# Optimization experiments

Measured on AMD Instinct MI355X. Metric: run time of the kernel, lower is better.

Reference implementation:

```python
import jax, jax.numpy as jnp
import numpy as np

VOCAB = 50257
CH = 1024          # c_hidden_size = hidden_size(1020) + class_num(4)
LAT = 128
T = 1024
EOS = 1


def setup_inputs() -> dict:
    key = jax.random.key(0)
    ks = jax.random.split(key, 12)
    s = 0.02
    # tokens in [2, VOCAB) so EOS only appears at the final position
    toks = jax.random.randint(ks[0], (T,), 2, VOCAB, dtype=jnp.int32)
    input_tensor = toks.at[-1].set(EOS)
    inp = {
        "input_tensor": input_tensor,
        "h0": jnp.zeros((1, 1, CH), jnp.float32),
        "c0": jnp.zeros((1, 1, CH), jnp.float32),
        "eps": jax.random.normal(ks[1], (1, 1, LAT), jnp.float32),
        "emb": jax.random.normal(ks[2], (VOCAB, CH), jnp.float32) * s,
        "W_ih": jax.random.normal(ks[3], (4 * CH, CH), jnp.float32) * s,
        "W_hh": jax.random.normal(ks[4], (4 * CH, CH), jnp.float32) * s,
        "b_ih": jax.random.normal(ks[5], (4 * CH,), jnp.float32) * s,
        "b_hh": jax.random.normal(ks[6], (4 * CH,), jnp.float32) * s,
        "W_mean": jax.random.normal(ks[7], (LAT, 2 * CH), jnp.float32) * s,
        "b_mean": jnp.zeros((LAT,), jnp.float32),
        "W_logv": jax.random.normal(ks[8], (LAT, 2 * CH), jnp.float32) * s,
        "b_logv": jnp.zeros((LAT,), jnp.float32),
    }
    return inp


def reference(input_tensor, h0, c0, eps, emb, W_ih, W_hh, b_ih, b_hh,
              W_mean, b_mean, W_logv, b_logv):
    Tlen = input_tensor.shape[0]
    eos_idx = jnp.argmax(input_tensor == EOS)           # first EOS position
    active = jnp.arange(Tlen) < eos_idx                 # steps taken before break
    x_all = emb[input_tensor]                            # [T, CH]

    def step(carry, inp):
        h, c = carry
        x, a = inp
        gates = x @ W_ih.T + b_ih + h @ W_hh.T + b_hh    # [4*CH]
        i, f, g, o = jnp.split(gates, 4)                 # PyTorch LSTM gate order
        c_new = jax.nn.sigmoid(f) * c + jax.nn.sigmoid(i) * jnp.tanh(g)
        h_new = jax.nn.sigmoid(o) * jnp.tanh(c_new)
        h = jnp.where(a, h_new, h)
        c = jnp.where(a, c_new, c)
        return (h, c), None

    (h, c), _ = jax.lax.scan(step, (h0.reshape(-1), c0.reshape(-1)), (x_all, active))
    hc = jnp.concatenate([h, c])                         # cat((h, c), dim=2) flattened
    mean = hc @ W_mean.T + b_mean
    logv = hc @ W_logv.T + b_logv
    z = eps.reshape(-1) * jnp.exp(0.5 * logv) + mean     # reparameterize
    shp = (1, 1, LAT)
    return z.reshape(shp), mean.reshape(shp), logv.reshape(shp)
```

## Files before the change

kernel.cpp:

```cpp
#include <hip/hip_runtime.h>
#include <cstdint>
#include <cstddef>

#define T_LEN 1024
#define CH    1024
#define NGATE 4096
#define LAT   128
#define NBLK  128

#define WS_HBUF  (16777216)
#define WS_HFIN  (16777216 + 16384)
#define WS_CFIN  (16777216 + 24576)

#define SWZ(j) ((j) ^ ((((j) >> 5) & 7) << 2))

__device__ __forceinline__ float sigmf(float x) { return 1.0f / (1.0f + expf(-x)); }

template <int CTRL, int RM>
__device__ __forceinline__ float dpp_add(float x) {
  int t = __builtin_amdgcn_update_dpp(0, __float_as_int(x), CTRL, RM, 0xf, true);
  return x + __int_as_float(t);
}

__device__ __forceinline__ float wave_sum63(float x) {
  x = dpp_add<0x111, 0xf>(x);
  x = dpp_add<0x112, 0xf>(x);
  x = dpp_add<0x114, 0xf>(x);
  x = dpp_add<0x118, 0xf>(x);
  x = dpp_add<0x142, 0xa>(x);
  x = dpp_add<0x143, 0xc>(x);
  return x;
}

__global__ __launch_bounds__(1024, 4) void lstm_k(const int* __restrict__ tok,
                                                  const float* __restrict__ h0,
                                                  const float* __restrict__ c0,
                                                  const float* __restrict__ eps,
                                                  const float* __restrict__ emb,
                                                  const float* __restrict__ Wih,
                                                  const float* __restrict__ Whh,
                                                  const float* __restrict__ bih,
                                                  const float* __restrict__ bhh,
                                                  const float* __restrict__ Wm,
                                                  const float* __restrict__ bm,
                                                  const float* __restrict__ Wl,
                                                  const float* __restrict__ bl,
                                                  unsigned long long* __restrict__ hbuf64,
                                                  unsigned long long* __restrict__ hfin64,
                                                  unsigned long long* __restrict__ cfin64,
                                                  float* __restrict__ out) {
  __shared__ float hs[1024];
  __shared__ float hcs[2048];
  __shared__ float4 gpart[16];
  __shared__ float rs[32];
  __shared__ int red[1024];

  const int tid = threadIdx.x;
  const int b = blockIdx.x;
  const int wv = tid >> 6;
  const int ln = tid & 63;
  const int dw = wv & 7;
  const int mb = (wv >> 3) * 2;
  const int kbase = ln * 16 + 4 * mb;
  const int hsw = SWZ(tid);
  const int swzmask = ((ln >> 1) & 7) << 2;
  const int idx0 = kbase ^ swzmask;
  const int idx1 = (kbase + 4) ^ swzmask;

  red[tid] = (tok[tid] == 1) ? tid : 0x7fffffff;
  __syncthreads();
  for (int s = 512; s > 0; s >>= 1) {
    if (tid < s) red[tid] = min(red[tid], red[tid + s]);
    __syncthreads();
  }
  const int e0 = red[0];
  const int eos = (e0 == 0x7fffffff) ? 0 : e0;
  __syncthreads();

  float4 w4[4][2];
  float4 wx[4][2];
#pragma unroll
  for (int q = 0; q < 4; q++) {
    const size_t roff = (size_t)(q * 1024 + b * 8 + dw) * CH + kbase;
    w4[q][0] = *(const float4*)(Whh + roff);
    w4[q][1] = *(const float4*)(Whh + roff + 4);
    wx[q][0] = *(const float4*)(Wih + roff);
    wx[q][1] = *(const float4*)(Wih + roff + 4);
  }

  float bias[4] = {0.f, 0.f, 0.f, 0.f};
  if (tid < 8) {
#pragma unroll
    for (int q = 0; q < 4; q++) {
      const int r = q * 1024 + b * 8 + tid;
      bias[q] = bih[r] + bhh[r];
    }
  }

  float hreg = 0.0f, creg = 0.0f;
  if (tid < 8) { hreg = h0[b * 8 + tid]; creg = c0[b * 8 + tid]; }

  for (int t = 0; t < eos; t++) {
    const int tokv = tok[t];
    const float* xrow = emb + (size_t)tokv * CH + kbase;
    const float4 x4a = *(const float4*)(xrow);
    const float4 x4b = *(const float4*)(xrow + 4);

    if (t == 0) {
      hs[hsw] = h0[tid];
    } else {
      const unsigned want = (unsigned)t;
      const unsigned long long* src = hbuf64 + (size_t)(t & 1) * 1024 + tid;
      unsigned long long v;
      do {
        v = __hip_atomic_load(src, __ATOMIC_RELAXED, __HIP_MEMORY_SCOPE_AGENT);
      } while ((unsigned)(v >> 32) != want);
      hs[hsw] = __uint_as_float((unsigned)(v & 0xffffffffu));
    }
    __syncthreads();

    float a0, a1, a2, a3;
    {
      a0 = wx[0][0].x * x4a.x + wx[0][0].y * x4a.y +
           wx[0][0].z * x4a.z + wx[0][0].w * x4a.w +
           wx[0][1].x * x4b.x + wx[0][1].y * x4b.y +
           wx[0][1].z * x4b.z + wx[0][1].w * x4b.w;
      a1 = wx[1][0].x * x4a.x + wx[1][0].y * x4a.y +
           wx[1][0].z * x4a.z + wx[1][0].w * x4a.w +
           wx[1][1].x * x4b.x + wx[1][1].y * x4b.y +
           wx[1][1].z * x4b.z + wx[1][1].w * x4b.w;
      a2 = wx[2][0].x * x4a.x + wx[2][0].y * x4a.y +
           wx[2][0].z * x4a.z + wx[2][0].w * x4a.w +
           wx[2][1].x * x4b.x + wx[2][1].y * x4b.y +
           wx[2][1].z * x4b.z + wx[2][1].w * x4b.w;
      a3 = wx[3][0].x * x4a.x + wx[3][0].y * x4a.y +
           wx[3][0].z * x4a.z + wx[3][0].w * x4a.w +
           wx[3][1].x * x4b.x + wx[3][1].y * x4b.y +
           wx[3][1].z * x4b.z + wx[3][1].w * x4b.w;
      const float4 h4a = *(const float4*)&hs[idx0];
      const float4 h4b = *(const float4*)&hs[idx1];
      a0 += w4[0][0].x * h4a.x; a0 += w4[0][0].y * h4a.y;
      a0 += w4[0][0].z * h4a.z; a0 += w4[0][0].w * h4a.w;
      a0 += w4[0][1].x * h4b.x; a0 += w4[0][1].y * h4b.y;
      a0 += w4[0][1].z * h4b.z; a0 += w4[0][1].w * h4b.w;
      a1 += w4[1][0].x * h4a.x; a1 += w4[1][0].y * h4a.y;
      a1 += w4[1][0].z * h4a.z; a1 += w4[1][0].w * h4a.w;
      a1 += w4[1][1].x * h4b.x; a1 += w4[1][1].y * h4b.y;
      a1 += w4[1][1].z * h4b.z; a1 += w4[1][1].w * h4b.w;
      a2 += w4[2][0].x * h4a.x; a2 += w4[2][0].y * h4a.y;
      a2 += w4[2][0].z * h4a.z; a2 += w4[2][0].w * h4a.w;
      a2 += w4[2][1].x * h4b.x; a2 += w4[2][1].y * h4b.y;
      a2 += w4[2][1].z * h4b.z; a2 += w4[2][1].w * h4b.w;
      a3 += w4[3][0].x * h4a.x; a3 += w4[3][0].y * h4a.y;
      a3 += w4[3][0].z * h4a.z; a3 += w4[3][0].w * h4a.w;
      a3 += w4[3][1].x * h4b.x; a3 += w4[3][1].y * h4b.y;
      a3 += w4[3][1].z * h4b.z; a3 += w4[3][1].w * h4b.w;
    }
    a0 = wave_sum63(a0);
    a1 = wave_sum63(a1);
    a2 = wave_sum63(a2);
    a3 = wave_sum63(a3);
    if (ln == 63) gpart[wv] = float4{a0, a1, a2, a3};
    __syncthreads();

    if (tid < 8) {
      const float4 g0 = gpart[tid];
      const float4 g1 = gpart[tid + 8];
      const float iv = g0.x + g1.x + bias[0];
      const float fv = g0.y + g1.y + bias[1];
      const float gg = g0.z + g1.z + bias[2];
      const float ov = g0.w + g1.w + bias[3];
      const float cn = sigmf(fv) * creg + sigmf(iv) * tanhf(gg);
      const float hn = sigmf(ov) * tanhf(cn);
      creg = cn; hreg = hn;
      const unsigned long long pv =
          ((unsigned long long)(unsigned)(t + 1) << 32) |
          (unsigned long long)__float_as_uint(hn);
      __hip_atomic_store(&hbuf64[(size_t)((t + 1) & 1) * 1024 + b * 8 + tid], pv,
                         __ATOMIC_RELAXED, __HIP_MEMORY_SCOPE_AGENT);
    }
  }

  if (tid < 8) {
    const unsigned long long ph = (1ull << 32) | (unsigned long long)__float_as_uint(hreg);
    const unsigned long long pc = (1ull << 32) | (unsigned long long)__float_as_uint(creg);
    __hip_atomic_store(&hfin64[b * 8 + tid], ph, __ATOMIC_RELAXED, __HIP_MEMORY_SCOPE_AGENT);
    __hip_atomic_store(&cfin64[b * 8 + tid], pc, __ATOMIC_RELAXED, __HIP_MEMORY_SCOPE_AGENT);
  }

  {
    unsigned long long vh, vc;
    do {
      vh = __hip_atomic_load(&hfin64[tid], __ATOMIC_RELAXED, __HIP_MEMORY_SCOPE_AGENT);
    } while ((unsigned)(vh >> 32) != 1u);
    do {
      vc = __hip_atomic_load(&cfin64[tid], __ATOMIC_RELAXED, __HIP_MEMORY_SCOPE_AGENT);
    } while ((unsigned)(vc >> 32) != 1u);
    hcs[tid] = __uint_as_float((unsigned)(vh & 0xffffffffu));
    hcs[1024 + tid] = __uint_as_float((unsigned)(vc & 0xffffffffu));
  }
  __syncthreads();

  float hc1 = hcs[tid];
  float hc2 = hcs[1024 + tid];
  float pm = Wm[(size_t)b * 2048 + tid] * hc1 + Wm[(size_t)b * 2048 + 1024 + tid] * hc2;
  float pl = Wl[(size_t)b * 2048 + tid] * hc1 + Wl[(size_t)b * 2048 + 1024 + tid] * hc2;
#pragma unroll
  for (int o = 32; o > 0; o >>= 1) {
    pm += __shfl_down(pm, o);
    pl += __shfl_down(pl, o);
  }
  if (ln == 0) { rs[wv] = pm; rs[16 + wv] = pl; }
  __syncthreads();
  if (tid == 0) {
    float m = 0.0f, l = 0.0f;
    for (int i = 0; i < 16; i++) { m += rs[i]; l += rs[16 + i]; }
    m += bm[b];
    l += bl[b];
    float z = eps[b] * expf(0.5f * l) + m;
    out[b] = z;
    out[LAT + b] = m;
    out[2 * LAT + b] = l;
  }
}

extern "C" void kernel_launch(void* const* d_in, const int* in_sizes, int n_in,
                              void* d_out, int out_size, void* d_ws, size_t ws_size,
                              hipStream_t stream) {
  const int*   tok = (const int*)d_in[0];
  const float* h0  = (const float*)d_in[1];
  const float* c0  = (const float*)d_in[2];
  const float* eps = (const float*)d_in[3];
  const float* emb = (const float*)d_in[4];
  const float* Wih = (const float*)d_in[5];
  const float* Whh = (const float*)d_in[6];
  const float* bih = (const float*)d_in[7];
  const float* bhh = (const float*)d_in[8];
  const float* Wm  = (const float*)d_in[9];
  const float* bm  = (const float*)d_in[10];
  const float* Wl  = (const float*)d_in[11];
  const float* bl  = (const float*)d_in[12];
  float* out = (float*)d_out;

  char* ws = (char*)d_ws;
  unsigned long long* hbuf64 = (unsigned long long*)(ws + WS_HBUF);
  unsigned long long* hfin64 = (unsigned long long*)(ws + WS_HFIN);
  unsigned long long* cfin64 = (unsigned long long*)(ws + WS_CFIN);

  void* args[] = {(void*)&tok, (void*)&h0, (void*)&c0, (void*)&eps,
                  (void*)&emb, (void*)&Wih, (void*)&Whh, (void*)&bih, (void*)&bhh,
                  (void*)&Wm, (void*)&bm, (void*)&Wl, (void*)&bl,
                  (void*)&hbuf64, (void*)&hfin64, (void*)&cfin64, (void*)&out};
  hipLaunchCooperativeKernel((void*)lstm_k, dim3(NBLK), dim3(1024), args, 0, stream);
}
```

Baseline: 2.363 ms.

## Halve block size so each wave owns one hidden unit, removing per-step cross-wave reduction

```diff
diff --git a/kernel.cpp b/kernel.cpp
--- a/kernel.cpp
+++ b/kernel.cpp
@@ -4,7 +4,6 @@
 
 #define T_LEN 1024
 #define CH    1024
-#define NGATE 4096
 #define LAT   128
 #define NBLK  128
 
@@ -12,9 +11,20 @@
 #define WS_HFIN  (16777216 + 16384)
 #define WS_CFIN  (16777216 + 24576)
 
-#define SWZ(j) ((j) ^ ((((j) >> 5) & 7) << 2))
-
-__device__ __forceinline__ float sigmf(float x) { return 1.0f / (1.0f + expf(-x)); }
+#define SWZ(j) ((j) ^ ((((j) >> 4) & 7) << 2))
+
+#define LOG2E 1.44269504088896340736f
+__device__ __forceinline__ float fsig(float x) {
+  return __builtin_amdgcn_rcpf(1.0f + __builtin_amdgcn_exp2f(-LOG2E * x));
+}
+__device__ __forceinline__ float ftanh(float x) {
+  float e = __builtin_amdgcn_exp2f(2.0f * LOG2E * x);
+  return 1.0f - 2.0f * __builtin_amdgcn_rcpf(e + 1.0f);
+}
+
+__device__ __forceinline__ float dot4(float4 a, float4 b) {
+  return a.x * b.x + a.y * b.y + a.z * b.z + a.w * b.w;
+}
 
 template <int CTRL, int RM>
 __device__ __forceinline__ float dpp_add(float x) {
@@ -32,44 +42,51 @@
   return x;
 }
 
-__global__ __launch_bounds__(1024, 4) void lstm_k(const int* __restrict__ tok,
-                                                  const float* __restrict__ h0,
-                                                  const float* __restrict__ c0,
-                                                  const float* __restrict__ eps,
-                                                  const float* __restrict__ emb,
-                                                  const float* __restrict__ Wih,
-                                                  const float* __restrict__ Whh,
-                                                  const float* __restrict__ bih,
-                                                  const float* __restrict__ bhh,
-                                                  const float* __restrict__ Wm,
-                                                  const float* __restrict__ bm,
-                                                  const float* __restrict__ Wl,
-                                                  const float* __restrict__ bl,
-                                                  unsigned long long* __restrict__ hbuf64,
-                                                  unsigned long long* __restrict__ hfin64,
-                                                  unsigned long long* __restrict__ cfin64,
-                                                  float* __restrict__ out) {
-  __shared__ float hs[1024];
+__device__ __forceinline__ unsigned long long apoll(const unsigned long long* p) {
+  return __hip_atomic_load(p, __ATOMIC_RELAXED, __HIP_MEMORY_SCOPE_AGENT);
+}
+__device__ __forceinline__ void apub(unsigned long long* p, unsigned tag, float v) {
+  const unsigned long long pv =
+      ((unsigned long long)tag << 32) | (unsigned long long)__float_as_uint(v);
+  __hip_atomic_store(p, pv, __ATOMIC_RELAXED, __HIP_MEMORY_SCOPE_AGENT);
+}
+
+__global__ __launch_bounds__(512, 2) void lstm_k(const int* __restrict__ tok,
+                                                 const float* __restrict__ h0,
+                                                 const float* __restrict__ c0,
+                                                 const float* __restrict__ eps,
+                                                 const float* __restrict__ emb,
+                                                 const float* __restrict__ Wih,
+                                                 const float* __restrict__ Whh,
+                                                 const float* __restrict__ bih,
+                                                 const float* __restrict__ bhh,
+                                                 const float* __restrict__ Wm,
+                                                 const float* __restrict__ bm,
+                                                 const float* __restrict__ Wl,
+                                                 const float* __restrict__ bl,
+                                                 unsigned long long* __restrict__ hbuf64,
+                                                 unsigned long long* __restrict__ hfin64,
+                                                 unsigned long long* __restrict__ cfin64,
+                                                 float* __restrict__ out) {
+  __shared__ float hs[2][1024];
   __shared__ float hcs[2048];
-  __shared__ float4 gpart[16];
-  __shared__ float rs[32];
-  __shared__ int red[1024];
+  __shared__ float rs[16];
+  __shared__ int red[512];
 
   const int tid = threadIdx.x;
   const int b = blockIdx.x;
   const int wv = tid >> 6;
   const int ln = tid & 63;
-  const int dw = wv & 7;
-  const int mb = (wv >> 3) * 2;
-  const int kbase = ln * 16 + 4 * mb;
-  const int hsw = SWZ(tid);
-  const int swzmask = ((ln >> 1) & 7) << 2;
-  const int idx0 = kbase ^ swzmask;
-  const int idx1 = (kbase + 4) ^ swzmask;
-
-  red[tid] = (tok[tid] == 1) ? tid : 0x7fffffff;
-  __syncthreads();
-  for (int s = 512; s > 0; s >>= 1) {
+  const int kbase = ln * 16;
+  const int swzm = (ln & 7) << 2;
+
+  {
+    int v0 = (tok[tid] == 1) ? tid : 0x7fffffff;
+    int v1 = (tok[tid + 512] == 1) ? (tid + 512) : 0x7fffffff;
+    red[tid] = min(v0, v1);
+  }
+  __syncthreads();
+  for (int s = 256; s > 0; s >>= 1) {
     if (tid < s) red[tid] = min(red[tid], red[tid + s]);
     __syncthreads();
   }
@@ -77,147 +94,127 @@
   const int eos = (e0 == 0x7fffffff) ? 0 : e0;
   __syncthreads();
 
-  float4 w4[4][2];
-  float4 wx[4][2];
+  float4 wh[4][4];
+  float4 wx[4][4];
 #pragma unroll
   for (int q = 0; q < 4; q++) {
-    const size_t roff = (size_t)(q * 1024 + b * 8 + dw) * CH + kbase;
-    w4[q][0] = *(const float4*)(Whh + roff);
-    w4[q][1] = *(const float4*)(Whh + roff + 4);
-    wx[q][0] = *(const float4*)(Wih + roff);
-    wx[q][1] = *(const float4*)(Wih + roff + 4);
-  }
-
-  float bias[4] = {0.f, 0.f, 0.f, 0.f};
-  if (tid < 8) {
-#pragma unroll
-    for (int q = 0; q < 4; q++) {
-      const int r = q * 1024 + b * 8 + tid;
-      bias[q] = bih[r] + bhh[r];
-    }
-  }
-
-  float hreg = 0.0f, creg = 0.0f;
-  if (tid < 8) { hreg = h0[b * 8 + tid]; creg = c0[b * 8 + tid]; }
+    const size_t roff = (size_t)(q * 1024 + b * 8 + wv) * CH + kbase;
+#pragma unroll
+    for (int m = 0; m < 4; m++) {
+      wh[q][m] = *(const float4*)(Whh + roff + 4 * m);
+      wx[q][m] = *(const float4*)(Wih + roff + 4 * m);
+    }
+  }
+
+  float bias0 = 0.f, bias1 = 0.f, bias2 = 0.f, bias3 = 0.f;
+  float hreg = 0.f, creg = 0.f;
+  if (ln == 63) {
+    const int d = b * 8 + wv;
+    bias0 = bih[d] + bhh[d];
+    bias1 = bih[1024 + d] + bhh[1024 + d];
+    bias2 = bih[2048 + d] + bhh[2048 + d];
+    bias3 = bih[3072 + d] + bhh[3072 + d];
+    hreg = h0[d];
+    creg = c0[d];
+  }
 
   for (int t = 0; t < eos; t++) {
-    const int tokv = tok[t];
-    const float* xrow = emb + (size_t)tokv * CH + kbase;
-    const float4 x4a = *(const float4*)(xrow);
-    const float4 x4b = *(const float4*)(xrow + 4);
+    const int pb = t & 1;
+
+    float a0, a1, a2, a3;
+    {
+      const float* xrow = emb + (size_t)tok[t] * CH + kbase;
+      float4 xv0 = *(const float4*)(xrow);
+      float4 xv1 = *(const float4*)(xrow + 4);
+      float4 xv2 = *(const float4*)(xrow + 8);
+      float4 xv3 = *(const float4*)(xrow + 12);
+      a0 = dot4(wx[0][0], xv0) + dot4(wx[0][1], xv1) +
+           dot4(wx[0][2], xv2) + dot4(wx[0][3], xv3);
+      a1 = dot4(wx[1][0], xv0) + dot4(wx[1][1], xv1) +
+           dot4(wx[1][2], xv2) + dot4(wx[1][3], xv3);
+      a2 = dot4(wx[2][0], xv0) + dot4(wx[2][1], xv1) +
+           dot4(wx[2][2], xv2) + dot4(wx[2][3], xv3);
+      a3 = dot4(wx[3][0], xv0) + dot4(wx[3][1], xv1) +
+           dot4(wx[3][2], xv2) + dot4(wx[3][3], xv3);
+    }
 
     if (t == 0) {
-      hs[hsw] = h0[tid];
+      hs[0][SWZ(2 * tid)] = h0[2 * tid];
+      hs[0][SWZ(2 * tid + 1)] = h0[2 * tid + 1];
     } else {
       const unsigned want = (unsigned)t;
-      const unsigned long long* src = hbuf64 + (size_t)(t & 1) * 1024 + tid;
-      unsigned long long v;
-      do {
-        v = __hip_atomic_load(src, __ATOMIC_RELAXED, __HIP_MEMORY_SCOPE_AGENT);
-      } while ((unsigned)(v >> 32) != want);
-      hs[hsw] = __uint_as_float((unsigned)(v & 0xffffffffu));
+      const unsigned long long* src = hbuf64 + (size_t)pb * 1024 + 2 * tid;
+      unsigned long long v0, v1;
+      do { v0 = apoll(src); } while ((unsigned)(v0 >> 32) != want);
+      do { v1 = apoll(src + 1); } while ((unsigned)(v1 >> 32) != want);
+      hs[pb][SWZ(2 * tid)] = __uint_as_float((unsigned)(v0 & 0xffffffffu));
+      hs[pb][SWZ(2 * tid + 1)] = __uint_as_float((unsigned)(v1 & 0xffffffffu));
     }
     __syncthreads();
 
-    float a0, a1, a2, a3;
-    {
-      a0 = wx[0][0].x * x4a.x + wx[0][0].y * x4a.y +
-           wx[0][0].z * x4a.z + wx[0][0].w * x4a.w +
-           wx[0][1].x * x4b.x + wx[0][1].y * x4b.y +
-           wx[0][1].z * x4b.z + wx[0][1].w * x4b.w;
-      a1 = wx[1][0].x * x4a.x + wx[1][0].y * x4a.y +
-           wx[1][0].z * x4a.z + wx[1][0].w * x4a.w +
-           wx[1][1].x * x4b.x + wx[1][1].y * x4b.y +
-           wx[1][1].z * x4b.z + wx[1][1].w * x4b.w;
-      a2 = wx[2][0].x * x4a.x + wx[2][0].y * x4a.y +
-           wx[2][0].z * x4a.z + wx[2][0].w * x4a.w +
-           wx[2][1].x * x4b.x + wx[2][1].y * x4b.y +
-           wx[2][1].z * x4b.z + wx[2][1].w * x4b.w;
-      a3 = wx[3][0].x * x4a.x + wx[3][0].y * x4a.y +
-           wx[3][0].z * x4a.z + wx[3][0].w * x4a.w +
-           wx[3][1].x * x4b.x + wx[3][1].y * x4b.y +
-           wx[3][1].z * x4b.z + wx[3][1].w * x4b.w;
-      const float4 h4a = *(const float4*)&hs[idx0];
-      const float4 h4b = *(const float4*)&hs[idx1];
-      a0 += w4[0][0].x * h4a.x; a0 += w4[0][0].y * h4a.y;
-      a0 += w4[0][0].z * h4a.z; a0 += w4[0][0].w * h4a.w;
-      a0 += w4[0][1].x * h4b.x; a0 += w4[0][1].y * h4b.y;
-      a0 += w4[0][1].z * h4b.z; a0 += w4[0][1].w * h4b.w;
-      a1 += w4[1][0].x * h4a.x; a1 += w4[1][0].y * h4a.y;
-      a1 += w4[1][0].z * h4a.z; a1 += w4[1][0].w * h4a.w;
-      a1 += w4[1][1].x * h4b.x; a1 += w4[1][1].y * h4b.y;
-      a1 += w4[1][1].z * h4b.z; a1 += w4[1][1].w * h4b.w;
-      a2 += w4[2][0].x * h4a.x; a2 += w4[2][0].y * h4a.y;
-      a2 += w4[2][0].z * h4a.z; a2 += w4[2][0].w * h4a.w;
-      a2 += w4[2][1].x * h4b.x; a2 += w4[2][1].y * h4b.y;
-      a2 += w4[2][1].z * h4b.z; a2 += w4[2][1].w * h4b.w;
-      a3 += w4[3][0].x * h4a.x; a3 += w4[3][0].y * h4a.y;
-      a3 += w4[3][0].z * h4a.z; a3 += w4[3][0].w * h4a.w;
-      a3 += w4[3][1].x * h4b.x; a3 += w4[3][1].y * h4b.y;
-      a3 += w4[3][1].z * h4b.z; a3 += w4[3][1].w * h4b.w;
+#pragma unroll
+    for (int m = 0; m < 4; m++) {
+      const float4 h4 = *(const float4*)&hs[pb][(kbase + 4 * m) ^ swzm];
+      a0 += dot4(wh[0][m], h4);
+      a1 += dot4(wh[1][m], h4);
+      a2 += dot4(wh[2][m], h4);
+      a3 += dot4(wh[3][m], h4);
     }
     a0 = wave_sum63(a0);
     a1 = wave_sum63(a1);
     a2 = wave_sum63(a2);
     a3 = wave_sum63(a3);
-    if (ln == 63) gpart[wv] = float4{a0, a1, a2, a3};
-    __syncthreads();
-
-    if (tid < 8) {
-      const float4 g0 = gpart[tid];
-      const float4 g1 = gpart[tid + 8];
-      const float iv = g0.x + g1.x + bias[0];
-      const float fv = g0.y + g1.y + bias[1];
-      const float gg = g0.z + g1.z + bias[2];
-      const float ov = g0.w + g1.w + bias[3];
-      const float cn = sigmf(fv) * creg + sigmf(iv) * tanhf(gg);
-      const float hn = sigmf(ov) * tanhf(cn);
+
+    if (ln == 63) {
+      const float iv = a0 + bias0, fv = a1 + bias1;
+      const float gg = a2 + bias2, ov = a3 + bias3;
+      const float cn = fsig(fv) * creg + fsig(iv) * ftanh(gg);
+      const float hn = fsig(ov) * ftanh(cn);
       creg = cn; hreg = hn;
-      const unsigned long long pv =
-          ((unsigned long long)(unsigned)(t + 1) << 32) |
-          (unsigned long long)__float_as_uint(hn);
-      __hip_atomic_store(&hbuf64[(size_t)((t + 1) & 1) * 1024 + b * 8 + tid], pv,
-                         __ATOMIC_RELAXED, __HIP_MEMORY_SCOPE_AGENT);
-    }
-  }
-
-  if (tid < 8) {
-    const unsigned long long ph = (1ull << 32) | (unsigned long long)__float_as_uint(hreg);
-    const unsigned long long pc = (1ull << 32) | (unsigned long long)__float_as_uint(creg);
-    __hip_atomic_store(&hfin64[b * 8 + tid], ph, __ATOMIC_RELAXED, __HIP_MEMORY_SCOPE_AGENT);
-    __hip_atomic_store(&cfin64[b * 8 + tid], pc, __ATOMIC_RELAXED, __HIP_MEMORY_SCOPE_AGENT);
+      apub(&hbuf64[(size_t)((t + 1) & 1) * 1024 + b * 8 + wv],
+           (unsigned)(t + 1), hn);
+    }
+  }
+
+  if (ln == 63) {
+    apub(&hfin64[b * 8 + wv], 1u, hreg);
+    apub(&cfin64[b * 8 + wv], 1u, creg);
   }
 
   {
-    unsigned long long vh, vc;
-    do {
-      vh = __hip_atomic_load(&hfin64[tid], __ATOMIC_RELAXED, __HIP_MEMORY_SCOPE_AGENT);
-    } while ((unsigned)(vh >> 32) != 1u);
-    do {
-      vc = __hip_atomic_load(&cfin64[tid], __ATOMIC_RELAXED, __HIP_MEMORY_SCOPE_AGENT);
-    } while ((unsigned)(vc >> 32) != 1u);
-    hcs[tid] = __uint_as_float((unsigned)(vh & 0xffffffffu));
-    hcs[1024 + tid] = __uint_as_float((unsigned)(vc & 0xffffffffu));
-  }
-  __syncthreads();
-
-  float hc1 = hcs[tid];
-  float hc2 = hcs[1024 + tid];
-  float pm = Wm[(size_t)b * 2048 + tid] * hc1 + Wm[(size_t)b * 2048 + 1024 + tid] * hc2;
-  float pl = Wl[(size_t)b * 2048 + tid] * hc1 + Wl[(size_t)b * 2048 + 1024 + tid] * hc2;
+#pragma unroll
+    for (int part = 0; part < 2; part++) {
+      const int i = tid + part * 512;
+      unsigned long long vh, vc;
+      do { vh = apoll(&hfin64[i]); } while ((unsigned)(vh >> 32) != 1u);
+      do { vc = apoll(&cfin64[i]); } while ((unsigned)(vc >> 32) != 1u);
+      hcs[i] = __uint_as_float((unsigned)(vh & 0xffffffffu));
+      hcs[1024 + i] = __uint_as_float((unsigned)(vc & 0xffffffffu));
+    }
+  }
+  __syncthreads();
+
+  float pm = 0.f, pl = 0.f;
+#pragma unroll
+  for (int part = 0; part < 4; part++) {
+    const int j = tid + part * 512;
+    const float hcv = hcs[j];
+    pm += Wm[(size_t)b * 2048 + j] * hcv;
+    pl += Wl[(size_t)b * 2048 + j] * hcv;
+  }
 #pragma unroll
   for (int o = 32; o > 0; o >>= 1) {
     pm += __shfl_down(pm, o);
     pl += __shfl_down(pl, o);
   }
-  if (ln == 0) { rs[wv] = pm; rs[16 + wv] = pl; }
+  if (ln == 0) { rs[wv] = pm; rs[8 + wv] = pl; }
   __syncthreads();
   if (tid == 0) {
     float m = 0.0f, l = 0.0f;
-    for (int i = 0; i < 16; i++) { m += rs[i]; l += rs[16 + i]; }
+    for (int i = 0; i < 8; i++) { m += rs[i]; l += rs[8 + i]; }
     m += bm[b];
     l += bl[b];
-    float z = eps[b] * expf(0.5f * l) + m;
+    const float z = eps[b] * expf(0.5f * l) + m;
     out[b] = z;
     out[LAT + b] = m;
     out[2 * LAT + b] = l;
@@ -247,9 +244,7 @@
   unsigned long long* hfin64 = (unsigned long long*)(ws + WS_HFIN);
   unsigned long long* cfin64 = (unsigned long long*)(ws + WS_CFIN);
 
-  void* args[] = {(void*)&tok, (void*)&h0, (void*)&c0, (void*)&eps,
-                  (void*)&emb, (void*)&Wih, (void*)&Whh, (void*)&bih, (void*)&bhh,
-                  (void*)&Wm, (void*)&bm, (void*)&Wl, (void*)&bl,
-                  (void*)&hbuf64, (void*)&hfin64, (void*)&cfin64, (void*)&out};
-  hipLaunchCooperativeKernel((void*)lstm_k, dim3(NBLK), dim3(1024), args, 0, stream);
-}
+  lstm_k<<<dim3(NBLK), dim3(512), 0, stream>>>(
+      tok, h0, c0, eps, emb, Wih, Whh, bih, bhh, Wm, bm, Wl, bl,
+      hbuf64, hfin64, cfin64, out);
+}
```

Measured after the change: 2.344 ms. No clear change (-0.8%).
